# Performance work log

Hardware: AMD Instinct MI355X
Metric: run time of the kernel (lower is better)

## Reference

```python
import jax, jax.numpy as jnp
import numpy as np

D_MODEL = 512
N_HEADS = 8
MAX_CH = 128
LN_EPS = 1e-5


def setup_inputs() -> dict:
    key = jax.random.key(0)
    ks = jax.random.split(key, 8)
    B, T, C, D = 8, 256, 64, D_MODEL
    x = jax.random.normal(ks[0], (B, T, C, D), dtype=jnp.float32)
    # nn.MultiheadAttention params: packed in_proj [3D, D], out_proj [D, D]
    in_proj_w = jax.random.normal(ks[1], (3 * D, D), dtype=jnp.float32) * 0.02
    in_proj_b = jnp.zeros((3 * D,), dtype=jnp.float32)
    out_proj_w = jax.random.normal(ks[2], (D, D), dtype=jnp.float32) * 0.02
    out_proj_b = jnp.zeros((D,), dtype=jnp.float32)
    ln_g = jnp.ones((D,), dtype=jnp.float32)
    ln_b = jnp.zeros((D,), dtype=jnp.float32)
    rel_pos_bias = jax.random.normal(ks[3], (N_HEADS, MAX_CH, MAX_CH), dtype=jnp.float32) * 0.02
    return {"x": x, "in_proj_w": in_proj_w, "in_proj_b": in_proj_b,
            "out_proj_w": out_proj_w, "out_proj_b": out_proj_b,
            "ln_g": ln_g, "ln_b": ln_b, "rel_pos_bias": rel_pos_bias}


def _layernorm(x, g, b):
    mu = jnp.mean(x, axis=-1, keepdims=True)
    var = jnp.var(x, axis=-1, keepdims=True)
    return (x - mu) * jax.lax.rsqrt(var + LN_EPS) * g + b


def reference(x, in_proj_w, in_proj_b, out_proj_w, out_proj_b, ln_g, ln_b, rel_pos_bias):
    B, T, C, D = x.shape
    H = N_HEADS
    hd = D // H
    N = B * T
    xf = x.reshape(N, C, D)
    # 2D additive attn_mask: mean over heads of rel-pos bias, broadcast over heads/batch
    bias = jnp.mean(rel_pos_bias[:, :C, :C], axis=0)  # [C, C]
    qkv = xf @ in_proj_w.T + in_proj_b  # [N, C, 3D]
    q, k, v = jnp.split(qkv, 3, axis=-1)
    q = q.reshape(N, C, H, hd)
    k = k.reshape(N, C, H, hd)
    v = v.reshape(N, C, H, hd)
    scores = jnp.einsum('nqhd,nkhd->nhqk', q, k) / jnp.sqrt(jnp.float32(hd))
    scores = scores + bias[None, None, :, :]
    attn = jax.nn.softmax(scores, axis=-1)
    ctx = jnp.einsum('nhqk,nkhd->nqhd', attn, v).reshape(N, C, D)
    attn_out = ctx @ out_proj_w.T + out_proj_b
    out = _layernorm(xf + attn_out, ln_g, ln_b)
    return out.reshape(B, T, C, D)
```

## Files before the change

kernel.cpp:

```cpp
#include <hip/hip_runtime.h>
#include <stdint.h>
#include <stddef.h>


typedef __attribute__((ext_vector_type(8))) short short8;
typedef __attribute__((ext_vector_type(4))) float f32x4;

typedef __attribute__((address_space(3))) unsigned int as3_u32;
typedef __attribute__((address_space(1))) unsigned int as1_u32;

#define VMCNT4 asm volatile("s_waitcnt vmcnt(4)" ::: "memory")
#define VMCNT0 asm volatile("s_waitcnt vmcnt(0)" ::: "memory")
#define LGKM0  asm volatile("s_waitcnt lgkmcnt(0)" ::: "memory")
#define BARR() __builtin_amdgcn_s_barrier()
#define PRIO1  __builtin_amdgcn_s_setprio(1)
#define PRIO0  __builtin_amdgcn_s_setprio(0)

__device__ __forceinline__ unsigned short f2bf(float f) {
  unsigned u = __builtin_bit_cast(unsigned, f);
  u = (u + 0x7FFFu + ((u >> 16) & 1u)) >> 16;
  return (unsigned short)u;
}

__device__ __forceinline__ f32x4 mfma16(short8 a, short8 b, f32x4 c) {
  return __builtin_amdgcn_mfma_f32_16x16x32_bf16(a, b, c, 0, 0, 0);
}

__device__ __forceinline__ short8 rd72(const char* buf, int row, int kelem) {
  return *(const short8*)(buf + row * 144 + kelem * 2);
}

__device__ __forceinline__ void stage4(char* ldsbase, const char* gsrc, int w, int lane) {
#pragma unroll
  for (int j = 0; j < 4; ++j) {
    int off = j * 4096 + w * 1024;
    __builtin_amdgcn_global_load_lds((const as1_u32*)(gsrc + off + lane * 16),
                                     (as3_u32*)(ldsbase + off), 16, 0, 0);
  }
}

__device__ __forceinline__ void qkv_chunk(const char* ws, const short8* xfp,
                                          int l15, int g, f32x4* acc) {
#pragma unroll
  for (int ks = 0; ks < 4; ++ks) {
    short8 a = xfp[ks];
#pragma unroll
    for (int nt = 0; nt < 4; ++nt) {
      int row = nt * 16 + l15;
      int kg = ks * 4 + g;
      int us = (kg & 8) | ((kg ^ row) & 7);
      short8 b = *(const short8*)(ws + row * 256 + us * 16);
      acc[nt] = mfma16(a, b, acc[nt]);
    }
  }
}

__device__ __forceinline__ void oproj_chunk(const char* ws, short8 af0, short8 af1,
                                            int l15, int g, f32x4* oaccp) {
#pragma unroll
  for (int nt2 = 0; nt2 < 8; ++nt2) {
    int row = nt2 * 16 + l15;
    int us0 = (g ^ row) & 7;
    int us1 = ((4 + g) ^ row) & 7;
    short8 b0 = *(const short8*)(ws + row * 128 + us0 * 16);
    oaccp[nt2] = mfma16(af0, b0, oaccp[nt2]);
    short8 b1 = *(const short8*)(ws + row * 128 + us1 * 16);
    oaccp[nt2] = mfma16(af1, b1, oaccp[nt2]);
  }
}

__global__ void prep_kernel(const float* __restrict__ wqkv_f,
                            const float* __restrict__ wo_f,
                            const float* __restrict__ rel,
                            unsigned short* __restrict__ wt,
                            float* __restrict__ bias2d) {
  int b = blockIdx.x, tid = threadIdx.x;
  if (b < 128) {
    int h = b >> 4, i = b & 15;
    unsigned short* dst = wt + (size_t)b * 8192;
#pragma unroll
    for (int t = 0; t < 4; ++t) {
      int u = t * 256 + tid;
      const float* src;
      if (i < 12) {
        int rg = i >> 2, kc = i & 3;
        int row = u >> 4, us = u & 15;
        int kg = (us & 8) | ((us ^ row) & 7);
        src = wqkv_f + (size_t)(rg * 512 + h * 64 + row) * 512 + kc * 128 + kg * 8;
      } else {
        int nc = i - 12;
        int row = u >> 3, us = u & 7;
        int kg = (us ^ row) & 7;
        src = wo_f + (size_t)(nc * 128 + row) * 512 + h * 64 + kg * 8;
      }
      float4 a = *(const float4*)src;
      float4 c = *(const float4*)(src + 4);
      unsigned p0 = (unsigned)f2bf(a.x) | ((unsigned)f2bf(a.y) << 16);
      unsigned p1 = (unsigned)f2bf(a.z) | ((unsigned)f2bf(a.w) << 16);
      unsigned p2 = (unsigned)f2bf(c.x) | ((unsigned)f2bf(c.y) << 16);
      unsigned p3 = (unsigned)f2bf(c.z) | ((unsigned)f2bf(c.w) << 16);
      *(uint4*)(dst + u * 8) = make_uint4(p0, p1, p2, p3);
    }
  } else {
    int idx = (b - 128) * 256 + tid;
    int m = idx >> 6, nn = idx & 63;
    float s = 0.f;
#pragma unroll
    for (int hh = 0; hh < 8; ++hh) s += rel[hh * 16384 + m * 128 + nn];
    bias2d[idx] = s * 0.125f;
  }
}

__global__ __launch_bounds__(256, 2) void attn_main(
    const float* __restrict__ x,
    const char* __restrict__ wq,
    const float* __restrict__ bqkv,
    const float* __restrict__ bo,
    const float* __restrict__ lng,
    const float* __restrict__ lnb,
    const float* __restrict__ bias2d,
    float* __restrict__ out) {
  __shared__ __attribute__((aligned(16))) char smem[51200];
  char* B0 = smem;
  char* B1 = smem + 9216;
  char* WSb = smem + 18432;

  const int n = blockIdx.x;
  const int tid = threadIdx.x;
  const int w = tid >> 6, lane = tid & 63;
  const int l15 = lane & 15, g = lane >> 4;
  const int mrow = w * 16 + g * 4;
  const int wrow = w * 16 + l15;

  float b2d[16];
#pragma unroll
  for (int nt = 0; nt < 4; ++nt)
#pragma unroll
    for (int r = 0; r < 4; ++r)
      b2d[nt * 4 + r] = bias2d[(mrow + r) * 64 + nt * 16 + l15];

  const float* xrow = x + ((size_t)n * 64 + wrow) * 512;
  short8 xf[16];
#pragma unroll
  for (int ks = 0; ks < 16; ++ks) {
    float4 a = *(const float4*)(xrow + ks * 32 + g * 8);
    float4 b = *(const float4*)(xrow + ks * 32 + g * 8 + 4);
    short8 s;
    s[0] = (short)f2bf(a.x); s[1] = (short)f2bf(a.y);
    s[2] = (short)f2bf(a.z); s[3] = (short)f2bf(a.w);
    s[4] = (short)f2bf(b.x); s[5] = (short)f2bf(b.y);
    s[6] = (short)f2bf(b.z); s[7] = (short)f2bf(b.w);
    xf[ks] = s;
  }

  f32x4 oacc[32] = {};

  stage4(WSb, wq, w, lane);

  for (int h = 0; h < 8; ++h) {
    const char* wh = wq + (size_t)h * 262144;
    {
      f32x4 qa[4] = {}; float bq[4];
#pragma unroll
      for (int i = 0; i < 4; ++i) {
        if (i == 3) {
#pragma unroll
          for (int nt = 0; nt < 4; ++nt) bq[nt] = bqkv[h * 64 + nt * 16 + l15];
        }
        stage4(WSb + (((i + 1) & 1) << 14), wh + (size_t)(i + 1) * 16384, w, lane);
        VMCNT4; BARR();
        PRIO1; qkv_chunk(WSb + ((i & 1) << 14), &xf[i * 4], l15, g, qa); PRIO0;
        if (i == 3) {
#pragma unroll
          for (int nt = 0; nt < 4; ++nt)
#pragma unroll
            for (int r = 0; r < 4; ++r)
              *(unsigned short*)(B0 + (mrow + r) * 144 + (nt * 16 + l15) * 2) =
                  f2bf(qa[nt][r] + bq[nt]);
        }
        LGKM0; BARR();
      }
    }
    {
      f32x4 ka[4] = {}; float bk[4];
#pragma unroll
      for (int i = 0; i < 4; ++i) {
        if (i == 3) {
#pragma unroll
          for (int nt = 0; nt < 4; ++nt) bk[nt] = bqkv[512 + h * 64 + nt * 16 + l15];
        }
        stage4(WSb + (((i + 1) & 1) << 14), wh + (size_t)(5 + i) * 16384, w, lane);
        VMCNT4; BARR();
        PRIO1; qkv_chunk(WSb + ((i & 1) << 14), &xf[i * 4], l15, g, ka); PRIO0;
        if (i == 3) {
#pragma unroll
          for (int nt = 0; nt < 4; ++nt)
#pragma unroll
            for (int r = 0; r < 4; ++r)
              *(unsigned short*)(B1 + (mrow + r) * 144 + (nt * 16 + l15) * 2) =
                  f2bf(ka[nt][r] + bk[nt]);
        }
        LGKM0; BARR();
      }
    }
    {
      f32x4 va[4] = {}; float bv[4];
#pragma unroll
      for (int i = 0; i < 4; ++i) {
        if (i == 3) {
#pragma unroll
          for (int nt = 0; nt < 4; ++nt) bv[nt] = bqkv[1024 + h * 64 + nt * 16 + l15];
        }
        stage4(WSb + (((i + 1) & 1) << 14), wh + (size_t)(9 + i) * 16384, w, lane);
        if (i == 0) {
          f32x4 sc[4] = {};
          short8 aq0 = rd72(B0, wrow, g * 8);
          short8 aq1 = rd72(B0, wrow, 32 + g * 8);
#pragma unroll
          for (int nt = 0; nt < 4; ++nt)
            sc[nt] = mfma16(aq0, rd72(B1, nt * 16 + l15, g * 8), sc[nt]);
#pragma unroll
          for (int nt = 0; nt < 4; ++nt)
            sc[nt] = mfma16(aq1, rd72(B1, nt * 16 + l15, 32 + g * 8), sc[nt]);
          float mx[4] = {-1e30f, -1e30f, -1e30f, -1e30f};
#pragma unroll
          for (int nt = 0; nt < 4; ++nt)
#pragma unroll
            for (int r = 0; r < 4; ++r) {
              float v = sc[nt][r] * 0.125f + b2d[nt * 4 + r];
              sc[nt][r] = v;
              mx[r] = fmaxf(mx[r], v);
            }
#pragma unroll
          for (int mk = 1; mk < 16; mk <<= 1)
#pragma unroll
            for (int r = 0; r < 4; ++r) mx[r] = fmaxf(mx[r], __shfl_xor(mx[r], mk));
          float sm[4] = {0.f, 0.f, 0.f, 0.f};
#pragma unroll
          for (int nt = 0; nt < 4; ++nt)
#pragma unroll
            for (int r = 0; r < 4; ++r) {
              float e = __expf(sc[nt][r] - mx[r]);
              sc[nt][r] = e;
              sm[r] += e;
            }
#pragma unroll
          for (int mk = 1; mk < 16; mk <<= 1)
#pragma unroll
            for (int r = 0; r < 4; ++r) sm[r] += __shfl_xor(sm[r], mk);
          float inv[4];
#pragma unroll
          for (int r = 0; r < 4; ++r) inv[r] = 1.0f / sm[r];
#pragma unroll
          for (int nt = 0; nt < 4; ++nt)
#pragma unroll
            for (int r = 0; r < 4; ++r)
              *(unsigned short*)(B0 + (mrow + r) * 144 + (nt * 16 + l15) * 2) =
                  f2bf(sc[nt][r] * inv[r]);
        }
        VMCNT4; BARR();
        PRIO1; qkv_chunk(WSb + ((i & 1) << 14), &xf[i * 4], l15, g, va); PRIO0;
        if (i == 3) {
#pragma unroll
          for (int nt = 0; nt < 4; ++nt) {
            unsigned short p0 = f2bf(va[nt][0] + bv[nt]);
            unsigned short p1 = f2bf(va[nt][1] + bv[nt]);
            unsigned short p2 = f2bf(va[nt][2] + bv[nt]);
            unsigned short p3 = f2bf(va[nt][3] + bv[nt]);
            unsigned lo = (unsigned)p0 | ((unsigned)p1 << 16);
            unsigned hi = (unsigned)p2 | ((unsigned)p3 << 16);
            *(uint2*)(B1 + (nt * 16 + l15) * 144 + mrow * 2) = make_uint2(lo, hi);
          }
        }
        LGKM0; BARR();
      }
    }
    {
      short8 af0, af1;
#pragma unroll
      for (int i = 0; i < 4; ++i) {
        bool dostage = (i < 3) || (h < 7);
        if (dostage)
          stage4(WSb + (((i + 1) & 1) << 14), wh + (size_t)(13 + i) * 16384, w, lane);
        if (i == 0) {
          f32x4 cv[4] = {};
          short8 ap0 = rd72(B0, wrow, g * 8);
          short8 ap1 = rd72(B0, wrow, 32 + g * 8);
#pragma unroll
          for (int nt = 0; nt < 4; ++nt)
            cv[nt] = mfma16(ap0, rd72(B1, nt * 16 + l15, g * 8), cv[nt]);
#pragma unroll
          for (int nt = 0; nt < 4; ++nt)
            cv[nt] = mfma16(ap1, rd72(B1, nt * 16 + l15, 32 + g * 8), cv[nt]);
#pragma unroll
          for (int nt = 0; nt < 4; ++nt)
#pragma unroll
            for (int r = 0; r < 4; ++r)
              *(unsigned short*)(B0 + (mrow + r) * 144 + (nt * 16 + l15) * 2) =
                  f2bf(cv[nt][r]);
        }
        if (dostage) { VMCNT4; } else { VMCNT0; }
        BARR();
        if (i == 0) {
          af0 = rd72(B0, wrow, g * 8);
          af1 = rd72(B0, wrow, 32 + g * 8);
        }
        PRIO1; oproj_chunk(WSb + ((i & 1) << 14), af0, af1, l15, g, &oacc[i * 8]); PRIO0;
        LGKM0; BARR();
      }
    }
  }

  float* EP = (float*)(smem + 18432);
  float s1[4] = {0.f, 0.f, 0.f, 0.f}, s2[4] = {0.f, 0.f, 0.f, 0.f};
  const float* xblk = x + (size_t)n * 32768;
  float* oblk = out + (size_t)n * 32768;
#pragma unroll
  for (int cc = 0; cc < 8; ++cc) {
#pragma unroll
    for (int t = 0; t < 4; ++t) {
      int flat = t * 256 + tid;
      int row = flat >> 4, f4 = flat & 15;
      float4 v = *(const float4*)(xblk + row * 512 + cc * 64 + f4 * 4);
      *(float4*)(EP + row * 68 + f4 * 4) = v;
    }
    __syncthreads();
#pragma unroll
    for (int i2 = 0; i2 < 4; ++i2) {
      int d = cc * 64 + i2 * 16 + l15;
      float bov = bo[d];
#pragma unroll
      for (int r = 0; r < 4; ++r) {
        float xv = EP[(mrow + r) * 68 + i2 * 16 + l15];
        float v = oacc[cc * 4 + i2][r] + bov + xv;
        oacc[cc * 4 + i2][r] = v;
        s1[r] += v;
        s2[r] += v * v;
      }
    }
    __syncthreads();
  }
#pragma unroll
  for (int mk = 1; mk < 16; mk <<= 1)
#pragma unroll
    for (int r = 0; r < 4; ++r) {
      s1[r] += __shfl_xor(s1[r], mk);
      s2[r] += __shfl_xor(s2[r], mk);
    }
  float mu[4], rs[4];
#pragma unroll
  for (int r = 0; r < 4; ++r) {
    mu[r] = s1[r] * (1.0f / 512.0f);
    float var = s2[r] * (1.0f / 512.0f) - mu[r] * mu[r];
    rs[r] = rsqrtf(var + 1e-5f);
  }
#pragma unroll
  for (int cc = 0; cc < 8; ++cc) {
#pragma unroll
    for (int i2 = 0; i2 < 4; ++i2) {
      int d = cc * 64 + i2 * 16 + l15;
      float gg = lng[d], bb = lnb[d];
#pragma unroll
      for (int r = 0; r < 4; ++r)
        EP[(mrow + r) * 68 + i2 * 16 + l15] =
            (oacc[cc * 4 + i2][r] - mu[r]) * rs[r] * gg + bb;
    }
    __syncthreads();
#pragma unroll
    for (int t = 0; t < 4; ++t) {
      int flat = t * 256 + tid;
      int row = flat >> 4, f4 = flat & 15;
      *(float4*)(oblk + row * 512 + cc * 64 + f4 * 4) =
          *(const float4*)(EP + row * 68 + f4 * 4);
    }
    __syncthreads();
  }
}

extern "C" void kernel_launch(void* const* d_in, const int* in_sizes, int n_in,
                              void* d_out, int out_size, void* d_ws, size_t ws_size,
                              hipStream_t stream) {
  const float* x    = (const float*)d_in[0];
  const float* wqkv = (const float*)d_in[1];
  const float* bqkv = (const float*)d_in[2];
  const float* wo   = (const float*)d_in[3];
  const float* bo   = (const float*)d_in[4];
  const float* lng  = (const float*)d_in[5];
  const float* lnb  = (const float*)d_in[6];
  const float* rel  = (const float*)d_in[7];

  unsigned short* wt = (unsigned short*)d_ws;
  float* bias2d = (float*)((char*)d_ws + 2097152);

  prep_kernel<<<144, 256, 0, stream>>>(wqkv, wo, rel, wt, bias2d);
  attn_main<<<2048, 256, 0, stream>>>(x, (const char*)d_ws, bqkv, bo, lng, lnb,
                                      bias2d, (float*)d_out);
}
```

Measured before the change: 621.3 us.

## Split fused attention into QKV/attention and out-projection+LayerNorm kernels with 2x2 warp tiling

Splits the single fused kernel into two. The first computes the QKV projection and per-head attention, writing a bf16 context tensor into the output buffer as scratch. The second does the out-projection, residual add and LayerNorm. Both GEMMs switch from one 16-row strip per warp to a 2x2 warp tiling, so each staged weight fragment feeds two MFMAs. The aim is to cut LDS weight reads per MFMA and to drop the 32 out-projection accumulators that were held live across all heads. The cost is an extra global round trip for the context tensor, an extra kernel launch, and reuse of the output buffer as scratch before the second kernel overwrites it.

```diff
diff --git a/kernel.cpp b/kernel.cpp
--- a/kernel.cpp
+++ b/kernel.cpp
@@ -9,6 +9,7 @@
 typedef __attribute__((address_space(3))) unsigned int as3_u32;
 typedef __attribute__((address_space(1))) unsigned int as1_u32;
 
+#define VMCNT5 asm volatile("s_waitcnt vmcnt(5)" ::: "memory")
 #define VMCNT4 asm volatile("s_waitcnt vmcnt(4)" ::: "memory")
 #define VMCNT0 asm volatile("s_waitcnt vmcnt(0)" ::: "memory")
 #define LGKM0  asm volatile("s_waitcnt lgkmcnt(0)" ::: "memory")
@@ -30,42 +31,12 @@
   return *(const short8*)(buf + row * 144 + kelem * 2);
 }
 
-__device__ __forceinline__ void stage4(char* ldsbase, const char* gsrc, int w, int lane) {
+__device__ __forceinline__ void stage16k(char* ldsbase, const char* gsrc, int w, int lane) {
 #pragma unroll
   for (int j = 0; j < 4; ++j) {
     int off = j * 4096 + w * 1024;
     __builtin_amdgcn_global_load_lds((const as1_u32*)(gsrc + off + lane * 16),
                                      (as3_u32*)(ldsbase + off), 16, 0, 0);
-  }
-}
-
-__device__ __forceinline__ void qkv_chunk(const char* ws, const short8* xfp,
-                                          int l15, int g, f32x4* acc) {
-#pragma unroll
-  for (int ks = 0; ks < 4; ++ks) {
-    short8 a = xfp[ks];
-#pragma unroll
-    for (int nt = 0; nt < 4; ++nt) {
-      int row = nt * 16 + l15;
-      int kg = ks * 4 + g;
-      int us = (kg & 8) | ((kg ^ row) & 7);
-      short8 b = *(const short8*)(ws + row * 256 + us * 16);
-      acc[nt] = mfma16(a, b, acc[nt]);
-    }
-  }
-}
-
-__device__ __forceinline__ void oproj_chunk(const char* ws, short8 af0, short8 af1,
-                                            int l15, int g, f32x4* oaccp) {
-#pragma unroll
-  for (int nt2 = 0; nt2 < 8; ++nt2) {
-    int row = nt2 * 16 + l15;
-    int us0 = (g ^ row) & 7;
-    int us1 = ((4 + g) ^ row) & 7;
-    short8 b0 = *(const short8*)(ws + row * 128 + us0 * 16);
-    oaccp[nt2] = mfma16(af0, b0, oaccp[nt2]);
-    short8 b1 = *(const short8*)(ws + row * 128 + us1 * 16);
-    oaccp[nt2] = mfma16(af1, b1, oaccp[nt2]);
   }
 }
 
@@ -76,22 +47,21 @@
                             float* __restrict__ bias2d) {
   int b = blockIdx.x, tid = threadIdx.x;
   if (b < 128) {
-    int h = b >> 4, i = b & 15;
     unsigned short* dst = wt + (size_t)b * 8192;
 #pragma unroll
     for (int t = 0; t < 4; ++t) {
       int u = t * 256 + tid;
+      int row = u >> 4, us = u & 15;
+      int kg = (us & 8) | ((us ^ row) & 7);
       const float* src;
-      if (i < 12) {
+      if (b < 96) {
+        int h = b / 12, i = b % 12;
         int rg = i >> 2, kc = i & 3;
-        int row = u >> 4, us = u & 15;
-        int kg = (us & 8) | ((us ^ row) & 7);
         src = wqkv_f + (size_t)(rg * 512 + h * 64 + row) * 512 + kc * 128 + kg * 8;
       } else {
-        int nc = i - 12;
-        int row = u >> 3, us = u & 7;
-        int kg = (us ^ row) & 7;
-        src = wo_f + (size_t)(nc * 128 + row) * 512 + h * 64 + kg * 8;
+        int cw = b - 96;
+        int kc = cw >> 3, ng = cw & 7;
+        src = wo_f + (size_t)(ng * 64 + row) * 512 + kc * 128 + kg * 8;
       }
       float4 a = *(const float4*)src;
       float4 c = *(const float4*)(src + 4);
@@ -111,24 +81,23 @@
   }
 }
 
-__global__ __launch_bounds__(256, 2) void attn_main(
+__global__ __launch_bounds__(256, 2) void attn_qkv(
     const float* __restrict__ x,
     const char* __restrict__ wq,
     const float* __restrict__ bqkv,
-    const float* __restrict__ bo,
-    const float* __restrict__ lng,
-    const float* __restrict__ lnb,
     const float* __restrict__ bias2d,
-    float* __restrict__ out) {
-  __shared__ __attribute__((aligned(16))) char smem[51200];
+    char* __restrict__ ctxg) {
+  __shared__ __attribute__((aligned(16))) char smem[60416];
   char* B0 = smem;
   char* B1 = smem + 9216;
-  char* WSb = smem + 18432;
+  char* B2 = smem + 18432;
+  char* WSb = smem + 27648;
 
   const int n = blockIdx.x;
   const int tid = threadIdx.x;
   const int w = tid >> 6, lane = tid & 63;
   const int l15 = lane & 15, g = lane >> 4;
+  const int wm = w >> 1, wn = w & 1;
   const int mrow = w * 16 + g * 4;
   const int wrow = w * 16 + l15;
 
@@ -139,241 +108,351 @@
     for (int r = 0; r < 4; ++r)
       b2d[nt * 4 + r] = bias2d[(mrow + r) * 64 + nt * 16 + l15];
 
-  const float* xrow = x + ((size_t)n * 64 + wrow) * 512;
-  short8 xf[16];
-#pragma unroll
-  for (int ks = 0; ks < 16; ++ks) {
-    float4 a = *(const float4*)(xrow + ks * 32 + g * 8);
-    float4 b = *(const float4*)(xrow + ks * 32 + g * 8 + 4);
-    short8 s;
-    s[0] = (short)f2bf(a.x); s[1] = (short)f2bf(a.y);
-    s[2] = (short)f2bf(a.z); s[3] = (short)f2bf(a.w);
-    s[4] = (short)f2bf(b.x); s[5] = (short)f2bf(b.y);
-    s[6] = (short)f2bf(b.z); s[7] = (short)f2bf(b.w);
-    xf[ks] = s;
-  }
-
-  f32x4 oacc[32] = {};
-
-  stage4(WSb, wq, w, lane);
-
+  stage16k(WSb, wq, w, lane);
+
+  short8 xf[32];
+#pragma unroll
+  for (int mt = 0; mt < 2; ++mt) {
+    const float* xr = x + ((size_t)n * 64 + wm * 32 + mt * 16 + l15) * 512;
+#pragma unroll
+    for (int kk = 0; kk < 16; ++kk) {
+      float4 a = *(const float4*)(xr + kk * 32 + g * 8);
+      float4 c = *(const float4*)(xr + kk * 32 + g * 8 + 4);
+      short8 s;
+      s[0] = (short)f2bf(a.x); s[1] = (short)f2bf(a.y);
+      s[2] = (short)f2bf(a.z); s[3] = (short)f2bf(a.w);
+      s[4] = (short)f2bf(c.x); s[5] = (short)f2bf(c.y);
+      s[6] = (short)f2bf(c.z); s[7] = (short)f2bf(c.w);
+      xf[mt * 16 + kk] = s;
+    }
+  }
+
+  int b = 0;
   for (int h = 0; h < 8; ++h) {
-    const char* wh = wq + (size_t)h * 262144;
-    {
-      f32x4 qa[4] = {}; float bq[4];
-#pragma unroll
-      for (int i = 0; i < 4; ++i) {
-        if (i == 3) {
-#pragma unroll
-          for (int nt = 0; nt < 4; ++nt) bq[nt] = bqkv[h * 64 + nt * 16 + l15];
-        }
-        stage4(WSb + (((i + 1) & 1) << 14), wh + (size_t)(i + 1) * 16384, w, lane);
-        VMCNT4; BARR();
-        PRIO1; qkv_chunk(WSb + ((i & 1) << 14), &xf[i * 4], l15, g, qa); PRIO0;
-        if (i == 3) {
-#pragma unroll
-          for (int nt = 0; nt < 4; ++nt)
+    float bq2[2], bk2[2], bv2[2];
+#pragma unroll
+    for (int nt = 0; nt < 2; ++nt) {
+      int col = h * 64 + wn * 32 + nt * 16 + l15;
+      bq2[nt] = bqkv[col];
+      bk2[nt] = bqkv[512 + col];
+      bv2[nt] = bqkv[1024 + col];
+    }
+#pragma unroll
+    for (int rg = 0; rg < 3; ++rg) {
+      f32x4 acc[2][2] = {};
+#pragma unroll
+      for (int c = 0; c < 4; ++c) {
+        if (b < 95)
+          stage16k(WSb + (((b + 1) & 1) << 14), wq + (size_t)(b + 1) * 16384, w, lane);
+        if (b < 95) { VMCNT4; } else { VMCNT0; }
+        BARR();
+        const char* ws = WSb + ((b & 1) << 14);
+        PRIO1;
+#pragma unroll
+        for (int ks = 0; ks < 4; ++ks) {
+#pragma unroll
+          for (int nt = 0; nt < 2; ++nt) {
+            int row = wn * 32 + nt * 16 + l15;
+            int kg = ks * 4 + g;
+            int us = (kg & 8) | ((kg ^ row) & 7);
+            short8 bfr = *(const short8*)(ws + row * 256 + us * 16);
+            acc[0][nt] = mfma16(xf[c * 4 + ks], bfr, acc[0][nt]);
+            acc[1][nt] = mfma16(xf[16 + c * 4 + ks], bfr, acc[1][nt]);
+          }
+        }
+        PRIO0;
+        LGKM0; BARR();
+        ++b;
+      }
+      if (rg == 0) {
+#pragma unroll
+        for (int mt = 0; mt < 2; ++mt)
+#pragma unroll
+          for (int nt = 0; nt < 2; ++nt)
 #pragma unroll
             for (int r = 0; r < 4; ++r)
-              *(unsigned short*)(B0 + (mrow + r) * 144 + (nt * 16 + l15) * 2) =
-                  f2bf(qa[nt][r] + bq[nt]);
-        }
-        LGKM0; BARR();
-      }
-    }
-    {
-      f32x4 ka[4] = {}; float bk[4];
-#pragma unroll
-      for (int i = 0; i < 4; ++i) {
-        if (i == 3) {
-#pragma unroll
-          for (int nt = 0; nt < 4; ++nt) bk[nt] = bqkv[512 + h * 64 + nt * 16 + l15];
-        }
-        stage4(WSb + (((i + 1) & 1) << 14), wh + (size_t)(5 + i) * 16384, w, lane);
-        VMCNT4; BARR();
-        PRIO1; qkv_chunk(WSb + ((i & 1) << 14), &xf[i * 4], l15, g, ka); PRIO0;
-        if (i == 3) {
-#pragma unroll
-          for (int nt = 0; nt < 4; ++nt)
+              *(unsigned short*)(B0 + (wm * 32 + mt * 16 + g * 4 + r) * 144 +
+                                 (wn * 32 + nt * 16 + l15) * 2) =
+                  f2bf(acc[mt][nt][r] + bq2[nt]);
+      } else if (rg == 1) {
+#pragma unroll
+        for (int mt = 0; mt < 2; ++mt)
+#pragma unroll
+          for (int nt = 0; nt < 2; ++nt)
 #pragma unroll
             for (int r = 0; r < 4; ++r)
-              *(unsigned short*)(B1 + (mrow + r) * 144 + (nt * 16 + l15) * 2) =
-                  f2bf(ka[nt][r] + bk[nt]);
-        }
-        LGKM0; BARR();
-      }
-    }
-    {
-      f32x4 va[4] = {}; float bv[4];
-#pragma unroll
-      for (int i = 0; i < 4; ++i) {
-        if (i == 3) {
-#pragma unroll
-          for (int nt = 0; nt < 4; ++nt) bv[nt] = bqkv[1024 + h * 64 + nt * 16 + l15];
-        }
-        stage4(WSb + (((i + 1) & 1) << 14), wh + (size_t)(9 + i) * 16384, w, lane);
-        if (i == 0) {
-          f32x4 sc[4] = {};
-          short8 aq0 = rd72(B0, wrow, g * 8);
-          short8 aq1 = rd72(B0, wrow, 32 + g * 8);
-#pragma unroll
-          for (int nt = 0; nt < 4; ++nt)
-            sc[nt] = mfma16(aq0, rd72(B1, nt * 16 + l15, g * 8), sc[nt]);
-#pragma unroll
-          for (int nt = 0; nt < 4; ++nt)
-            sc[nt] = mfma16(aq1, rd72(B1, nt * 16 + l15, 32 + g * 8), sc[nt]);
-          float mx[4] = {-1e30f, -1e30f, -1e30f, -1e30f};
-#pragma unroll
-          for (int nt = 0; nt < 4; ++nt)
-#pragma unroll
-            for (int r = 0; r < 4; ++r) {
-              float v = sc[nt][r] * 0.125f + b2d[nt * 4 + r];
-              sc[nt][r] = v;
-              mx[r] = fmaxf(mx[r], v);
-            }
-#pragma unroll
-          for (int mk = 1; mk < 16; mk <<= 1)
-#pragma unroll
-            for (int r = 0; r < 4; ++r) mx[r] = fmaxf(mx[r], __shfl_xor(mx[r], mk));
-          float sm[4] = {0.f, 0.f, 0.f, 0.f};
-#pragma unroll
-          for (int nt = 0; nt < 4; ++nt)
-#pragma unroll
-            for (int r = 0; r < 4; ++r) {
-              float e = __expf(sc[nt][r] - mx[r]);
-              sc[nt][r] = e;
-              sm[r] += e;
-            }
-#pragma unroll
-          for (int mk = 1; mk < 16; mk <<= 1)
-#pragma unroll
-            for (int r = 0; r < 4; ++r) sm[r] += __shfl_xor(sm[r], mk);
-          float inv[4];
-#pragma unroll
-          for (int r = 0; r < 4; ++r) inv[r] = 1.0f / sm[r];
-#pragma unroll
-          for (int nt = 0; nt < 4; ++nt)
-#pragma unroll
-            for (int r = 0; r < 4; ++r)
-              *(unsigned short*)(B0 + (mrow + r) * 144 + (nt * 16 + l15) * 2) =
-                  f2bf(sc[nt][r] * inv[r]);
-        }
-        VMCNT4; BARR();
-        PRIO1; qkv_chunk(WSb + ((i & 1) << 14), &xf[i * 4], l15, g, va); PRIO0;
-        if (i == 3) {
-#pragma unroll
-          for (int nt = 0; nt < 4; ++nt) {
-            unsigned short p0 = f2bf(va[nt][0] + bv[nt]);
-            unsigned short p1 = f2bf(va[nt][1] + bv[nt]);
-            unsigned short p2 = f2bf(va[nt][2] + bv[nt]);
-            unsigned short p3 = f2bf(va[nt][3] + bv[nt]);
+              *(unsigned short*)(B1 + (wm * 32 + mt * 16 + g * 4 + r) * 144 +
+                                 (wn * 32 + nt * 16 + l15) * 2) =
+                  f2bf(acc[mt][nt][r] + bk2[nt]);
+      } else {
+#pragma unroll
+        for (int mt = 0; mt < 2; ++mt)
+#pragma unroll
+          for (int nt = 0; nt < 2; ++nt) {
+            unsigned short p0 = f2bf(acc[mt][nt][0] + bv2[nt]);
+            unsigned short p1 = f2bf(acc[mt][nt][1] + bv2[nt]);
+            unsigned short p2 = f2bf(acc[mt][nt][2] + bv2[nt]);
+            unsigned short p3 = f2bf(acc[mt][nt][3] + bv2[nt]);
             unsigned lo = (unsigned)p0 | ((unsigned)p1 << 16);
             unsigned hi = (unsigned)p2 | ((unsigned)p3 << 16);
-            *(uint2*)(B1 + (nt * 16 + l15) * 144 + mrow * 2) = make_uint2(lo, hi);
+            *(uint2*)(B2 + (wn * 32 + nt * 16 + l15) * 144 +
+                      (wm * 32 + mt * 16 + g * 4) * 2) = make_uint2(lo, hi);
           }
-        }
-        LGKM0; BARR();
-      }
-    }
+      }
+    }
+    LGKM0; BARR();
+
     {
-      short8 af0, af1;
-#pragma unroll
-      for (int i = 0; i < 4; ++i) {
-        bool dostage = (i < 3) || (h < 7);
-        if (dostage)
-          stage4(WSb + (((i + 1) & 1) << 14), wh + (size_t)(13 + i) * 16384, w, lane);
-        if (i == 0) {
-          f32x4 cv[4] = {};
-          short8 ap0 = rd72(B0, wrow, g * 8);
-          short8 ap1 = rd72(B0, wrow, 32 + g * 8);
-#pragma unroll
-          for (int nt = 0; nt < 4; ++nt)
-            cv[nt] = mfma16(ap0, rd72(B1, nt * 16 + l15, g * 8), cv[nt]);
-#pragma unroll
-          for (int nt = 0; nt < 4; ++nt)
-            cv[nt] = mfma16(ap1, rd72(B1, nt * 16 + l15, 32 + g * 8), cv[nt]);
-#pragma unroll
-          for (int nt = 0; nt < 4; ++nt)
-#pragma unroll
-            for (int r = 0; r < 4; ++r)
-              *(unsigned short*)(B0 + (mrow + r) * 144 + (nt * 16 + l15) * 2) =
-                  f2bf(cv[nt][r]);
-        }
-        if (dostage) { VMCNT4; } else { VMCNT0; }
-        BARR();
-        if (i == 0) {
-          af0 = rd72(B0, wrow, g * 8);
-          af1 = rd72(B0, wrow, 32 + g * 8);
-        }
-        PRIO1; oproj_chunk(WSb + ((i & 1) << 14), af0, af1, l15, g, &oacc[i * 8]); PRIO0;
-        LGKM0; BARR();
-      }
-    }
-  }
-
-  float* EP = (float*)(smem + 18432);
-  float s1[4] = {0.f, 0.f, 0.f, 0.f}, s2[4] = {0.f, 0.f, 0.f, 0.f};
+      f32x4 sc[4] = {};
+      short8 aq0 = rd72(B0, wrow, g * 8);
+      short8 aq1 = rd72(B0, wrow, 32 + g * 8);
+#pragma unroll
+      for (int nt = 0; nt < 4; ++nt)
+        sc[nt] = mfma16(aq0, rd72(B1, nt * 16 + l15, g * 8), sc[nt]);
+#pragma unroll
+      for (int nt = 0; nt < 4; ++nt)
+        sc[nt] = mfma16(aq1, rd72(B1, nt * 16 + l15, 32 + g * 8), sc[nt]);
+      float mx[4] = {-1e30f, -1e30f, -1e30f, -1e30f};
+#pragma unroll
+      for (int nt = 0; nt < 4; ++nt)
+#pragma unroll
+        for (int r = 0; r < 4; ++r) {
+          float v = sc[nt][r] * 0.125f + b2d[nt * 4 + r];
+          sc[nt][r] = v;
+          mx[r] = fmaxf(mx[r], v);
+        }
+#pragma unroll
+      for (int mk = 1; mk < 16; mk <<= 1)
+#pragma unroll
+        for (int r = 0; r < 4; ++r) mx[r] = fmaxf(mx[r], __shfl_xor(mx[r], mk));
+      float sm[4] = {0.f, 0.f, 0.f, 0.f};
+#pragma unroll
+      for (int nt = 0; nt < 4; ++nt)
+#pragma unroll
+        for (int r = 0; r < 4; ++r) {
+          float e = __expf(sc[nt][r] - mx[r]);
+          sc[nt][r] = e;
+          sm[r] += e;
+        }
+#pragma unroll
+      for (int mk = 1; mk < 16; mk <<= 1)
+#pragma unroll
+        for (int r = 0; r < 4; ++r) sm[r] += __shfl_xor(sm[r], mk);
+      float inv[4];
+#pragma unroll
+      for (int r = 0; r < 4; ++r) inv[r] = 1.0f / sm[r];
+#pragma unroll
+      for (int nt = 0; nt < 4; ++nt)
+#pragma unroll
+        for (int r = 0; r < 4; ++r)
+          *(unsigned short*)(B0 + (mrow + r) * 144 + (nt * 16 + l15) * 2) =
+              f2bf(sc[nt][r] * inv[r]);
+    }
+
+    f32x4 cv[4] = {};
+    {
+      short8 ap0 = rd72(B0, wrow, g * 8);
+      short8 ap1 = rd72(B0, wrow, 32 + g * 8);
+#pragma unroll
+      for (int nt = 0; nt < 4; ++nt)
+        cv[nt] = mfma16(ap0, rd72(B2, nt * 16 + l15, g * 8), cv[nt]);
+#pragma unroll
+      for (int nt = 0; nt < 4; ++nt)
+        cv[nt] = mfma16(ap1, rd72(B2, nt * 16 + l15, 32 + g * 8), cv[nt]);
+    }
+    LGKM0; BARR();
+#pragma unroll
+    for (int nt = 0; nt < 4; ++nt)
+#pragma unroll
+      for (int r = 0; r < 4; ++r)
+        *(unsigned short*)(B2 + (mrow + r) * 144 + (nt * 16 + l15) * 2) =
+            f2bf(cv[nt][r]);
+    LGKM0; BARR();
+
+    {
+      char* cdst = ctxg + (size_t)n * 131072 + (h >> 1) * 16384 + (h & 1) * 128;
+#pragma unroll
+      for (int it = 0; it < 2; ++it) {
+        int flat = it * 256 + tid;
+        int row = flat >> 3, uu = flat & 7;
+        uint4 v = *(const uint4*)(B2 + row * 144 + uu * 16);
+        int slot = uu ^ (row & 7);
+        *(uint4*)(cdst + row * 256 + slot * 16) = v;
+      }
+    }
+  }
+}
+
+__global__ __launch_bounds__(256, 2) void oproj_ln(
+    const char* __restrict__ ctxg,
+    const char* __restrict__ wo,
+    const float* __restrict__ bo,
+    const float* __restrict__ x,
+    const float* __restrict__ lng,
+    const float* __restrict__ lnb,
+    float* __restrict__ out) {
+  __shared__ __attribute__((aligned(16))) char smem[65536];
+  char* WB = smem;
+  char* CB = smem + 32768;
+  float* EP  = (float*)smem;
+  float* SM1 = (float*)(smem + 32768);
+  float* SM2 = (float*)(smem + 33408);
+
+  const int n = blockIdx.x;
+  const int tid = threadIdx.x;
+  const int w = tid >> 6, lane = tid & 63;
+  const int l15 = lane & 15, g = lane >> 4;
+  const int um = w >> 1, un = w & 1;
+
+  const char* cbase = ctxg + (size_t)n * 131072;
+
+  stage16k(CB, cbase, w, lane);
+  stage16k(WB, wo, w, lane);
+
+  f32x4 acc[8][2][2] = {};
+
+  for (int kc = 0; kc < 4; ++kc) {
+    short8 actx[2][4];
+#pragma unroll
+    for (int ng = 0; ng < 8; ++ng) {
+      int b = kc * 8 + ng;
+      if (b < 31)
+        stage16k(WB + (((b + 1) & 1) << 14), wo + (size_t)(b + 1) * 16384, w, lane);
+      if ((ng & 1) == 0 && kc < 3) {
+        int p = ng >> 1;
+        int off = p * 4096 + w * 1024;
+        __builtin_amdgcn_global_load_lds(
+            (const as1_u32*)(cbase + (kc + 1) * 16384 + off + lane * 16),
+            (as3_u32*)(CB + (((kc + 1) & 1) << 14) + off), 16, 0, 0);
+      }
+      if (b < 31) { VMCNT5; } else { VMCNT0; }
+      BARR();
+      const char* cb = CB + ((kc & 1) << 14);
+      if (ng == 0) {
+#pragma unroll
+        for (int mt = 0; mt < 2; ++mt)
+#pragma unroll
+          for (int ks = 0; ks < 4; ++ks) {
+            int row = um * 32 + mt * 16 + l15;
+            int u = ks * 4 + g;
+            int us = u ^ (row & 7);
+            actx[mt][ks] = *(const short8*)(cb + row * 256 + us * 16);
+          }
+      }
+      const char* ws = WB + ((b & 1) << 14);
+      PRIO1;
+#pragma unroll
+      for (int ks = 0; ks < 4; ++ks) {
+#pragma unroll
+        for (int nt = 0; nt < 2; ++nt) {
+          int row = un * 32 + nt * 16 + l15;
+          int kg = ks * 4 + g;
+          int us = (kg & 8) | ((kg ^ row) & 7);
+          short8 bfr = *(const short8*)(ws + row * 256 + us * 16);
+          acc[ng][0][nt] = mfma16(actx[0][ks], bfr, acc[ng][0][nt]);
+          acc[ng][1][nt] = mfma16(actx[1][ks], bfr, acc[ng][1][nt]);
+        }
+      }
+      PRIO0;
+      LGKM0; BARR();
+    }
+  }
+
+  VMCNT0;
   const float* xblk = x + (size_t)n * 32768;
   float* oblk = out + (size_t)n * 32768;
-#pragma unroll
-  for (int cc = 0; cc < 8; ++cc) {
+  float s1[2][4] = {}, s2[2][4] = {};
+
+#pragma unroll
+  for (int ng = 0; ng < 8; ++ng) {
 #pragma unroll
     for (int t = 0; t < 4; ++t) {
       int flat = t * 256 + tid;
       int row = flat >> 4, f4 = flat & 15;
-      float4 v = *(const float4*)(xblk + row * 512 + cc * 64 + f4 * 4);
+      float4 v = *(const float4*)(xblk + row * 512 + ng * 64 + f4 * 4);
       *(float4*)(EP + row * 68 + f4 * 4) = v;
     }
-    __syncthreads();
-#pragma unroll
-    for (int i2 = 0; i2 < 4; ++i2) {
-      int d = cc * 64 + i2 * 16 + l15;
-      float bov = bo[d];
+    LGKM0; BARR();
+    float boA[2];
+#pragma unroll
+    for (int nt = 0; nt < 2; ++nt) boA[nt] = bo[ng * 64 + un * 32 + nt * 16 + l15];
+#pragma unroll
+    for (int mt = 0; mt < 2; ++mt)
+#pragma unroll
+      for (int nt = 0; nt < 2; ++nt)
+#pragma unroll
+        for (int r = 0; r < 4; ++r) {
+          int row = um * 32 + mt * 16 + g * 4 + r;
+          float xv = EP[row * 68 + un * 32 + nt * 16 + l15];
+          float v = acc[ng][mt][nt][r] + boA[nt] + xv;
+          acc[ng][mt][nt][r] = v;
+          s1[mt][r] += v;
+          s2[mt][r] += v * v;
+        }
+    LGKM0; BARR();
+  }
+#pragma unroll
+  for (int mk = 1; mk < 16; mk <<= 1)
+#pragma unroll
+    for (int mt = 0; mt < 2; ++mt)
 #pragma unroll
       for (int r = 0; r < 4; ++r) {
-        float xv = EP[(mrow + r) * 68 + i2 * 16 + l15];
-        float v = oacc[cc * 4 + i2][r] + bov + xv;
-        oacc[cc * 4 + i2][r] = v;
-        s1[r] += v;
-        s2[r] += v * v;
-      }
-    }
-    __syncthreads();
-  }
-#pragma unroll
-  for (int mk = 1; mk < 16; mk <<= 1)
+        s1[mt][r] += __shfl_xor(s1[mt][r], mk);
+        s2[mt][r] += __shfl_xor(s2[mt][r], mk);
+      }
+  if (l15 == 0) {
+#pragma unroll
+    for (int mt = 0; mt < 2; ++mt)
+#pragma unroll
+      for (int r = 0; r < 4; ++r) {
+        int row = um * 32 + mt * 16 + g * 4 + r;
+        SM1[row * 2 + un] = s1[mt][r];
+        SM2[row * 2 + un] = s2[mt][r];
+      }
+  }
+  LGKM0; BARR();
+  float mu[2][4], rs[2][4];
+#pragma unroll
+  for (int mt = 0; mt < 2; ++mt)
 #pragma unroll
     for (int r = 0; r < 4; ++r) {
-      s1[r] += __shfl_xor(s1[r], mk);
-      s2[r] += __shfl_xor(s2[r], mk);
-    }
-  float mu[4], rs[4];
-#pragma unroll
-  for (int r = 0; r < 4; ++r) {
-    mu[r] = s1[r] * (1.0f / 512.0f);
-    float var = s2[r] * (1.0f / 512.0f) - mu[r] * mu[r];
-    rs[r] = rsqrtf(var + 1e-5f);
-  }
-#pragma unroll
-  for (int cc = 0; cc < 8; ++cc) {
-#pragma unroll
-    for (int i2 = 0; i2 < 4; ++i2) {
-      int d = cc * 64 + i2 * 16 + l15;
-      float gg = lng[d], bb = lnb[d];
-#pragma unroll
-      for (int r = 0; r < 4; ++r)
-        EP[(mrow + r) * 68 + i2 * 16 + l15] =
-            (oacc[cc * 4 + i2][r] - mu[r]) * rs[r] * gg + bb;
-    }
-    __syncthreads();
+      int row = um * 32 + mt * 16 + g * 4 + r;
+      float a1 = SM1[row * 2] + SM1[row * 2 + 1];
+      float a2 = SM2[row * 2] + SM2[row * 2 + 1];
+      float m = a1 * (1.0f / 512.0f);
+      float var = a2 * (1.0f / 512.0f) - m * m;
+      mu[mt][r] = m;
+      rs[mt][r] = rsqrtf(var + 1e-5f);
+    }
+  BARR();
+#pragma unroll
+  for (int ng = 0; ng < 8; ++ng) {
+    float lgA[2], lbA[2];
+#pragma unroll
+    for (int nt = 0; nt < 2; ++nt) {
+      int col = ng * 64 + un * 32 + nt * 16 + l15;
+      lgA[nt] = lng[col];
+      lbA[nt] = lnb[col];
+    }
+#pragma unroll
+    for (int mt = 0; mt < 2; ++mt)
+#pragma unroll
+      for (int nt = 0; nt < 2; ++nt)
+#pragma unroll
+        for (int r = 0; r < 4; ++r) {
+          int row = um * 32 + mt * 16 + g * 4 + r;
+          EP[row * 68 + un * 32 + nt * 16 + l15] =
+              (acc[ng][mt][nt][r] - mu[mt][r]) * rs[mt][r] * lgA[nt] + lbA[nt];
+        }
+    LGKM0; BARR();
 #pragma unroll
     for (int t = 0; t < 4; ++t) {
       int flat = t * 256 + tid;
       int row = flat >> 4, f4 = flat & 15;
-      *(float4*)(oblk + row * 512 + cc * 64 + f4 * 4) =
+      *(float4*)(oblk + row * 512 + ng * 64 + f4 * 4) =
           *(const float4*)(EP + row * 68 + f4 * 4);
     }
-    __syncthreads();
+    BARR();
   }
 }
 
@@ -390,9 +469,12 @@
   const float* rel  = (const float*)d_in[7];
 
   unsigned short* wt = (unsigned short*)d_ws;
-  float* bias2d = (float*)((char*)d_ws + 2097152);
+  float* bias2d = (float*)((char*)d_ws + 128 * 16384);
+  const char* wqc = (const char*)d_ws;
+  const char* woc = (const char*)d_ws + 96 * 16384;
 
   prep_kernel<<<144, 256, 0, stream>>>(wqkv, wo, rel, wt, bias2d);
-  attn_main<<<2048, 256, 0, stream>>>(x, (const char*)d_ws, bqkv, bo, lng, lnb,
-                                      bias2d, (float*)d_out);
-}
+  attn_qkv<<<2048, 256, 0, stream>>>(x, wqc, bqkv, bias2d, (char*)d_out);
+  oproj_ln<<<2048, 256, 0, stream>>>((const char*)d_out, woc, bo, x, lng, lnb,
+                                     (float*)d_out);
+}
```

After: 578.2 us. -6.9%, faster.
